# Kernel tuning notes

Hardware: AMD Instinct MI355X
Metric: run time of the kernel (lower is better)

## Reference

```python
import jax, jax.numpy as jnp
import numpy as np


def setup_inputs() -> dict:
    key = jax.random.key(0)
    k1, k2 = jax.random.split(key)
    B, C, L = 32, 512, 2048
    x = jax.random.normal(k1, (B, C, L), dtype=jnp.float32)
    # learned smoothing coefficient per channel, init like torch.full(..., 0.3)
    alpha = jnp.full((1, C), 0.3, dtype=jnp.float32)
    return {"x": x, "alpha": alpha}


def _ema(x, alpha):
    # x: [B, C, L], alpha: [1, C]
    # reg[..., 0] = x[..., 0]; reg[..., i] = (1-a)*reg[..., i-1] + a*x[..., i]
    xt = jnp.moveaxis(x, -1, 0)  # [L, B, C]

    def step(pre, x_i):
        new = (1.0 - alpha) * pre + alpha * x_i  # broadcast (1,C) over (B,C)
        return new, new

    init = xt[0]
    _, ys = jax.lax.scan(step, init, xt[1:])  # [L-1, B, C]
    out = jnp.concatenate([xt[:1], ys], axis=0)  # [L, B, C]
    return jnp.moveaxis(out, 0, -1)  # [B, C, L]


def reference(x, alpha):
    return _ema(x, alpha)
```

## Files before the change

kernel.cpp:

```cpp
#include <hip/hip_runtime.h>


#define ROW_LEN 2048
#define NROUND 8
#define WAVES_PER_BLOCK 4

__global__ __launch_bounds__(256)
void ema_rows_kernel(const float* __restrict__ x,
                     const float* __restrict__ alpha,
                     float* __restrict__ out,
                     int C, int nrows) {
    const int wave = threadIdx.x >> 6;
    const int lane = threadIdx.x & 63;
    const int row = blockIdx.x * WAVES_PER_BLOCK + wave;
    if (row >= nrows) return;

    const float a = alpha[row % C];
    const float cm = 1.0f - a;
    const float cm2 = cm * cm;
    const float cm3 = cm2 * cm;
    const float cm4 = cm2 * cm2;

    const float4* __restrict__ xv =
        reinterpret_cast<const float4*>(x + (size_t)row * ROW_LEN);
    float4* __restrict__ ov =
        reinterpret_cast<float4*>(out + (size_t)row * ROW_LEN);

    float4 v[NROUND];
    #pragma unroll
    for (int j = 0; j < NROUND; ++j) v[j] = xv[j * 64 + lane];

    float carry = 0.0f;

    #pragma unroll
    for (int j = 0; j < NROUND; ++j) {
        float p0 = a * v[j].x;
        if (j == 0 && lane == 0) p0 = v[j].x;
        float p1 = fmaf(cm, p0, a * v[j].y);
        float p2 = fmaf(cm, p1, a * v[j].z);
        float p3 = fmaf(cm, p2, a * v[j].w);

        float A = (j == 0 && lane == 0) ? 0.0f : cm4;
        float Bv = p3;

        #pragma unroll
        for (int off = 1; off < 64; off <<= 1) {
            float Ap = __shfl_up(A, off, 64);
            float Bp = __shfl_up(Bv, off, 64);
            if (lane >= off) {
                Bv = fmaf(A, Bp, Bv);
                A = A * Ap;
            }
        }

        float S = fmaf(A, carry, Bv);
        float Sin = __shfl_up(S, 1, 64);
        if (lane == 0) Sin = carry;

        float4 y;
        y.x = fmaf(cm,  Sin, p0);
        y.y = fmaf(cm2, Sin, p1);
        y.z = fmaf(cm3, Sin, p2);
        y.w = fmaf(cm4, Sin, p3);

        ov[j * 64 + lane] = y;

        carry = __shfl(S, 63, 64);
    }
}

extern "C" void kernel_launch(void* const* d_in, const int* in_sizes, int n_in,
                              void* d_out, int out_size, void* d_ws, size_t ws_size,
                              hipStream_t stream) {
    const float* x = (const float*)d_in[0];
    const float* alpha = (const float*)d_in[1];
    float* out = (float*)d_out;

    const int C = in_sizes[1];
    const int nrows = in_sizes[0] / ROW_LEN;

    const int blocks = (nrows + WAVES_PER_BLOCK - 1) / WAVES_PER_BLOCK;
    ema_rows_kernel<<<blocks, 64 * WAVES_PER_BLOCK, 0, stream>>>(x, alpha, out, C, nrows);
}
```

Measured before the change: 44.34 us.

## Use constant-decay prefix scan batched across rounds with closed-form carry propagation

The wave-level scan now relies on the decay being a per-channel constant, so it precomputes powers of (1-a) and drops the A-multiplier shuffles, halving the shuffle count. All eight rounds are scanned together with interleaved shuffles, which raises instruction-level parallelism. The serial carry is then applied through per-lane decay powers and cm^256. Stores switch to nontemporal. This keeps more values live in registers, and the products of powers could change float rounding slightly.

New measurement: 44.29 us. Within noise of the previous version (-0.1%).

```diff
diff --git a/kernel.cpp b/kernel.cpp
--- a/kernel.cpp
+++ b/kernel.cpp
@@ -1,5 +1,7 @@
 #include <hip/hip_runtime.h>
 
+
+typedef float vfloat4 __attribute__((ext_vector_type(4)));
 
 #define ROW_LEN 2048
 #define NROUND 8
@@ -15,23 +17,36 @@
     const int row = blockIdx.x * WAVES_PER_BLOCK + wave;
     if (row >= nrows) return;
 
-    const float a = alpha[row % C];
+    const float a  = alpha[row % C];
     const float cm = 1.0f - a;
-    const float cm2 = cm * cm;
-    const float cm3 = cm2 * cm;
-    const float cm4 = cm2 * cm2;
+    const float cm2 = cm * cm, cm3 = cm2 * cm, cm4 = cm2 * cm2;
+    const float m1  = cm4;
+    const float m2  = m1 * m1;
+    const float m4  = m2 * m2;
+    const float m8  = m4 * m4;
+    const float m16 = m8 * m8;
+    const float m32 = m16 * m16;
+    const float cm256 = m32 * m32;
 
-    const float4* __restrict__ xv =
-        reinterpret_cast<const float4*>(x + (size_t)row * ROW_LEN);
-    float4* __restrict__ ov =
-        reinterpret_cast<float4*>(out + (size_t)row * ROW_LEN);
+    float cmp4l = 1.0f;
+    if (lane & 1)  cmp4l *= m1;
+    if (lane & 2)  cmp4l *= m2;
+    if (lane & 4)  cmp4l *= m4;
+    if (lane & 8)  cmp4l *= m8;
+    if (lane & 16) cmp4l *= m16;
+    if (lane & 32) cmp4l *= m32;
 
-    float4 v[NROUND];
+    const vfloat4* __restrict__ xv =
+        reinterpret_cast<const vfloat4*>(x + (size_t)row * ROW_LEN);
+    vfloat4* __restrict__ ov =
+        reinterpret_cast<vfloat4*>(out + (size_t)row * ROW_LEN);
+
+    vfloat4 v[NROUND];
     #pragma unroll
     for (int j = 0; j < NROUND; ++j) v[j] = xv[j * 64 + lane];
 
-    float carry = 0.0f;
-
+    float p[NROUND][4];
+    float Bh[NROUND];
     #pragma unroll
     for (int j = 0; j < NROUND; ++j) {
         float p0 = a * v[j].x;
@@ -39,33 +54,41 @@
         float p1 = fmaf(cm, p0, a * v[j].y);
         float p2 = fmaf(cm, p1, a * v[j].z);
         float p3 = fmaf(cm, p2, a * v[j].w);
+        p[j][0] = p0; p[j][1] = p1; p[j][2] = p2; p[j][3] = p3;
+        Bh[j] = p3;
+    }
 
-        float A = (j == 0 && lane == 0) ? 0.0f : cm4;
-        float Bv = p3;
+    #pragma unroll
+    for (int s = 0; s < 6; ++s) {
+        const int off = 1 << s;
+        const float mult = (s == 0) ? m1 : (s == 1) ? m2 : (s == 2) ? m4
+                         : (s == 3) ? m8 : (s == 4) ? m16 : m32;
+        #pragma unroll
+        for (int j = 0; j < NROUND; ++j) {
+            float Bp = __shfl_up(Bh[j], off, 64);
+            if (lane >= off) Bh[j] = fmaf(mult, Bp, Bh[j]);
+        }
+    }
 
-        #pragma unroll
-        for (int off = 1; off < 64; off <<= 1) {
-            float Ap = __shfl_up(A, off, 64);
-            float Bp = __shfl_up(Bv, off, 64);
-            if (lane >= off) {
-                Bv = fmaf(A, Bp, Bv);
-                A = A * Ap;
-            }
-        }
+    float Bhp[NROUND], B63[NROUND];
+    #pragma unroll
+    for (int j = 0; j < NROUND; ++j) {
+        float t = __shfl_up(Bh[j], 1, 64);
+        Bhp[j] = (lane == 0) ? 0.0f : t;
+        B63[j] = __shfl(Bh[j], 63, 64);
+    }
 
-        float S = fmaf(A, carry, Bv);
-        float Sin = __shfl_up(S, 1, 64);
-        if (lane == 0) Sin = carry;
-
-        float4 y;
-        y.x = fmaf(cm,  Sin, p0);
-        y.y = fmaf(cm2, Sin, p1);
-        y.z = fmaf(cm3, Sin, p2);
-        y.w = fmaf(cm4, Sin, p3);
-
-        ov[j * 64 + lane] = y;
-
-        carry = __shfl(S, 63, 64);
+    float carry = 0.0f;
+    #pragma unroll
+    for (int j = 0; j < NROUND; ++j) {
+        const float Sin = fmaf(cmp4l, carry, Bhp[j]);
+        vfloat4 y;
+        y.x = fmaf(cm,  Sin, p[j][0]);
+        y.y = fmaf(cm2, Sin, p[j][1]);
+        y.z = fmaf(cm3, Sin, p[j][2]);
+        y.w = fmaf(cm4, Sin, p[j][3]);
+        __builtin_nontemporal_store(y, &ov[j * 64 + lane]);
+        carry = fmaf(cm256, carry, B63[j]);
     }
 }
 
```
